# Optimization experiments

Measured on AMD Instinct MI355X. Metric: run time of the kernel, lower is better.

## Reference

```python
import jax, jax.numpy as jnp
import numpy as np
from jax import lax

WIN = 9
PAD = WIN // 2


def _box_sum(x):
    # x: [B,1,H,W]; all-ones WINxWIN conv, stride 1, pad PAD -> same spatial size
    k = jnp.ones((1, 1, WIN, WIN), dtype=x.dtype)
    return lax.conv_general_dilated(
        x, k, window_strides=(1, 1), padding=[(PAD, PAD), (PAD, PAD)],
        dimension_numbers=("NCHW", "OIHW", "NCHW"))


def setup_inputs() -> dict:
    key = jax.random.key(0)
    k1, k2 = jax.random.split(key)
    B, C, H, W = 32, 1, 512, 512
    y_true = jax.random.uniform(k1, (B, C, H, W), dtype=jnp.float32)
    y_pred = jax.random.uniform(k2, (B, C, H, W), dtype=jnp.float32)
    return {"y_true": y_true, "y_pred": y_pred}


def reference(y_true, y_pred):
    Ii, Ji = y_true, y_pred
    win_size = float(WIN * WIN)
    I_sum = _box_sum(Ii)
    J_sum = _box_sum(Ji)
    I2_sum = _box_sum(Ii * Ii)
    J2_sum = _box_sum(Ji * Ji)
    IJ_sum = _box_sum(Ii * Ji)
    u_I = I_sum / win_size
    u_J = J_sum / win_size
    cross = IJ_sum - u_J * I_sum - u_I * J_sum + u_I * u_J * win_size
    I_var = I2_sum - 2.0 * u_I * I_sum + u_I * u_I * win_size
    J_var = J2_sum - 2.0 * u_J * J_sum + u_J * u_J * win_size
    cc = cross * cross / (I_var * J_var + 1e-05)
    return -jnp.mean(cc)
```

## Files before the change

### kernel.cpp

```cpp
#include <hip/hip_runtime.h>


#define BATCH   32
#define IMH     512
#define IMW     512
#define SH      16
#define NSTRIP  32
#define NPART   (BATCH * NSTRIP)
#define NK      24
#define VROW    520

#define PREFG(KK, PI, PJ) do {                                             \
    const int kk_ = (KK);                                                  \
    const int ri_ = r0 - 4 + kk_;                                          \
    PI = make_float2(0.f, 0.f); PJ = make_float2(0.f, 0.f);                \
    if (kk_ < NK && (unsigned)ri_ < (unsigned)IMH) {                       \
        PI = *(const float2*)(Ib + (size_t)ri_ * IMW + c0);                \
        PJ = *(const float2*)(Jb + (size_t)ri_ * IMW + c0);                \
    }                                                                      \
} while (0)

#define HWIN(QI, HA, HB) do {                                              \
    const float2 w0_ = *(const float2*)&Vbuf[QI][c0];                      \
    const float2 w1_ = *(const float2*)&Vbuf[QI][c0 + 2];                  \
    const float2 w2_ = *(const float2*)&Vbuf[QI][c0 + 4];                  \
    const float2 w3_ = *(const float2*)&Vbuf[QI][c0 + 6];                  \
    const float2 w4_ = *(const float2*)&Vbuf[QI][c0 + 8];                  \
    HA = ((w0_.x + w0_.y) + (w1_.x + w1_.y))                               \
       + ((w2_.x + w2_.y) + (w3_.x + w3_.y)) + w4_.x;                      \
    HB = HA + w4_.y - w0_.x;                                               \
} while (0)

#define CC1(AI, AJ, S2, S3, S4) do {                                       \
    const float cross = (S4) - (AI)*(AJ)*inv81;                            \
    const float ivv   = (S2) - (AI)*(AI)*inv81;                            \
    const float jvv   = (S3) - (AJ)*(AJ)*inv81;                            \
    acc += cross * cross * __builtin_amdgcn_rcpf(ivv * jvv + 1e-5f);       \
} while (0)

#define EMIT() do {                                                        \
    *(float2*)&Vbuf[0][4 + c0] = make_float2(VI0, VI1);                    \
    *(float2*)&Vbuf[1][4 + c0] = make_float2(VJ0, VJ1);                    \
    *(float2*)&Vbuf[2][4 + c0] = make_float2(VA0, VA1);                    \
    *(float2*)&Vbuf[3][4 + c0] = make_float2(VB0, VB1);                    \
    *(float2*)&Vbuf[4][4 + c0] = make_float2(VC0, VC1);                    \
    __syncthreads();                                                       \
    float HI0, HI1, HJ0, HJ1, HA0, HA1, HB0, HB1, HC0, HC1;                \
    HWIN(0, HI0, HI1);                                                     \
    HWIN(1, HJ0, HJ1);                                                     \
    HWIN(2, HA0, HA1);                                                     \
    HWIN(3, HB0, HB1);                                                     \
    HWIN(4, HC0, HC1);                                                     \
    CC1(HI0, HJ0, HA0, HB0, HC0);                                          \
    CC1(HI1, HJ1, HA1, HB1, HC1);                                          \
    __syncthreads();      \
} while (0)

#define BODY(K, PI, PJ) do {                                               \
    float4 oldv = make_float4(0.f, 0.f, 0.f, 0.f);                         \
    if ((K) >= 9) oldv = ring[slot][t];                                    \
    ring[slot][t] = make_float4(PI.x, PI.y, PJ.x, PJ.y);                   \
    slot = (slot == 8) ? 0 : slot + 1;                                     \
    VI0 += PI.x - oldv.x;             VI1 += PI.y - oldv.y;                \
    VJ0 += PJ.x - oldv.z;             VJ1 += PJ.y - oldv.w;                \
    VA0 += PI.x*PI.x - oldv.x*oldv.x; VA1 += PI.y*PI.y - oldv.y*oldv.y;    \
    VB0 += PJ.x*PJ.x - oldv.z*oldv.z; VB1 += PJ.y*PJ.y - oldv.w*oldv.w;    \
    VC0 += PI.x*PJ.x - oldv.x*oldv.z; VC1 += PI.y*PJ.y - oldv.y*oldv.w;    \
    if ((K) >= 8) { EMIT(); }                                              \
} while (0)

__global__ __launch_bounds__(256, 4) void ncc_main(const float* __restrict__ I,
                                                   const float* __restrict__ J,
                                                   float* __restrict__ partial) {
    const int t  = threadIdx.x;
    const int s  = blockIdx.x;
    const int b  = blockIdx.y;
    const int r0 = s * SH;
    const int c0 = 2 * t;
    const float inv81 = 1.0f / 81.0f;

    const float* Ib = I + (size_t)b * IMH * IMW;
    const float* Jb = J + (size_t)b * IMH * IMW;

    __shared__ float  Vbuf[5][VROW];
    __shared__ float4 ring[9][256];

    if (t < 40) {
        const int q = t >> 3, p = t & 7;
        Vbuf[q][p < 4 ? p : 512 + p] = 0.f;
    }
    __syncthreads();

    float VI0 = 0.f, VI1 = 0.f, VJ0 = 0.f, VJ1 = 0.f;
    float VA0 = 0.f, VA1 = 0.f, VB0 = 0.f, VB1 = 0.f;
    float VC0 = 0.f, VC1 = 0.f;
    float acc = 0.f;
    int slot = 0;

    float2 pa_i, pa_j, pb_i, pb_j, pc_i, pc_j, pd_i, pd_j;
    PREFG(0, pa_i, pa_j);
    PREFG(1, pb_i, pb_j);
    PREFG(2, pc_i, pc_j);
    PREFG(3, pd_i, pd_j);

#pragma unroll 1
    for (int g = 0; g < 6; ++g) {
        const int K = 4 * g;
        BODY(K,     pa_i, pa_j);  PREFG(K + 4, pa_i, pa_j);
        BODY(K + 1, pb_i, pb_j);  PREFG(K + 5, pb_i, pb_j);
        BODY(K + 2, pc_i, pc_j);  PREFG(K + 6, pc_i, pc_j);
        BODY(K + 3, pd_i, pd_j);  PREFG(K + 7, pd_i, pd_j);
    }

    float sum = acc;
#pragma unroll
    for (int off = 32; off > 0; off >>= 1) sum += __shfl_down(sum, off, 64);

    __shared__ float wsum[4];
    if ((t & 63) == 0) wsum[t >> 6] = sum;
    __syncthreads();
    if (t == 0) {
        partial[(size_t)b * NSTRIP + s] = wsum[0] + wsum[1] + wsum[2] + wsum[3];
    }
}

__global__ __launch_bounds__(256) void ncc_reduce(const float* __restrict__ partial,
                                                  float* __restrict__ out) {
    const int t = threadIdx.x;
    double ssum = 0.0;
    for (int idx = t; idx < NPART; idx += 256) ssum += (double)partial[idx];
#pragma unroll
    for (int off = 32; off > 0; off >>= 1) ssum += __shfl_down(ssum, off, 64);

    __shared__ double wsum[4];
    if ((t & 63) == 0) wsum[t >> 6] = ssum;
    __syncthreads();
    if (t == 0) {
        const double total = wsum[0] + wsum[1] + wsum[2] + wsum[3];
        out[0] = (float)(-total / 8388608.0);
    }
}

extern "C" void kernel_launch(void* const* d_in, const int* in_sizes, int n_in,
                              void* d_out, int out_size, void* d_ws, size_t ws_size,
                              hipStream_t stream) {
    const float* I = (const float*)d_in[0];
    const float* J = (const float*)d_in[1];
    float* partial = (float*)d_ws;
    float* out     = (float*)d_out;

    dim3 grid(NSTRIP, BATCH);
    ncc_main<<<grid, 256, 0, stream>>>(I, J, partial);
    ncc_reduce<<<1, 256, 0, stream>>>(partial, out);
}
```

Baseline: 117.3 us.

## Use single-wavefront blocks with shuffle-based horizontal box sums

Each block becomes one 64-lane wavefront where every lane owns 8 contiguous columns. The horizontal 9-tap window sums are now built from per-lane prefix and suffix sums plus cross-lane shuffles, replacing the shared-memory staging buffer and the two block barriers per output row. Global loads widen to float4. The trade-off is only 1024 single-wave blocks, which means lower occupancy and less latency hiding, higher register pressure, and a prefetch depth cut from 4 rows to 2.

```diff
diff --git a/kernel.cpp b/kernel.cpp
--- a/kernel.cpp
+++ b/kernel.cpp
@@ -1,126 +1,152 @@
 #include <hip/hip_runtime.h>
 
 
-#define BATCH   32
-#define IMH     512
-#define IMW     512
-#define SH      16
-#define NSTRIP  32
-#define NPART   (BATCH * NSTRIP)
-#define NK      24
-#define VROW    520
+#define BATCH     32
+#define IMH       512
+#define IMW       512
+#define SH        16
+#define NROWSTRIP 32
+#define NK        (SH + 8)
+#define NPART     (BATCH * NROWSTRIP)
 
-#define PREFG(KK, PI, PJ) do {                                             \
+#define PREFG(KK, ILO, IHI, JLO, JHI) do {                                 \
     const int kk_ = (KK);                                                  \
     const int ri_ = r0 - 4 + kk_;                                          \
-    PI = make_float2(0.f, 0.f); PJ = make_float2(0.f, 0.f);                \
+    ILO = z4; IHI = z4; JLO = z4; JHI = z4;                                \
     if (kk_ < NK && (unsigned)ri_ < (unsigned)IMH) {                       \
-        PI = *(const float2*)(Ib + (size_t)ri_ * IMW + c0);                \
-        PJ = *(const float2*)(Jb + (size_t)ri_ * IMW + c0);                \
+        const float* rI_ = Ib + (size_t)ri_ * IMW + c0;                    \
+        const float* rJ_ = Jb + (size_t)ri_ * IMW + c0;                    \
+        ILO = *(const float4*)(rI_);                                       \
+        IHI = *(const float4*)(rI_ + 4);                                   \
+        JLO = *(const float4*)(rJ_);                                       \
+        JHI = *(const float4*)(rJ_ + 4);                                   \
     }                                                                      \
 } while (0)
 
-#define HWIN(QI, HA, HB) do {                                              \
-    const float2 w0_ = *(const float2*)&Vbuf[QI][c0];                      \
-    const float2 w1_ = *(const float2*)&Vbuf[QI][c0 + 2];                  \
-    const float2 w2_ = *(const float2*)&Vbuf[QI][c0 + 4];                  \
-    const float2 w3_ = *(const float2*)&Vbuf[QI][c0 + 6];                  \
-    const float2 w4_ = *(const float2*)&Vbuf[QI][c0 + 8];                  \
-    HA = ((w0_.x + w0_.y) + (w1_.x + w1_.y))                               \
-       + ((w2_.x + w2_.y) + (w3_.x + w3_.y)) + w4_.x;                      \
-    HB = HA + w4_.y - w0_.x;                                               \
+#define HQ(LO, HI_, H0, H1, H2, H3, H4, H5, H6, H7) do {                   \
+    const float P0 = (LO).x, P1 = P0 + (LO).y,                             \
+                P2 = P1 + (LO).z, P3 = P2 + (LO).w;                        \
+    const float P4 = P3 + (HI_).x, P5 = P4 + (HI_).y,                      \
+                P6 = P5 + (HI_).z, P7 = P6 + (HI_).w;                      \
+    const float S1 = (HI_).w, S2 = (HI_).z + S1,                           \
+                S3 = (HI_).y + S2, S4 = (HI_).x + S3;                      \
+    float ls4 = __shfl(S4, u - 1, 64), ls3 = __shfl(S3, u - 1, 64);        \
+    float ls2 = __shfl(S2, u - 1, 64), ls1 = __shfl(S1, u - 1, 64);        \
+    float rp1 = __shfl(P0, u + 1, 64), rp2 = __shfl(P1, u + 1, 64);        \
+    float rp3 = __shfl(P2, u + 1, 64), rp4 = __shfl(P3, u + 1, 64);        \
+    if (u == 0)  { ls4 = 0.f; ls3 = 0.f; ls2 = 0.f; ls1 = 0.f; }           \
+    if (u == 63) { rp1 = 0.f; rp2 = 0.f; rp3 = 0.f; rp4 = 0.f; }           \
+    H0 = ls4 + P4;        H1 = ls3 + P5;                                   \
+    H2 = ls2 + P6;        H3 = ls1 + P7;                                   \
+    H4 = P7 + rp1;        H5 = (P7 - P0) + rp2;                            \
+    H6 = (P7 - P1) + rp3; H7 = (P7 - P2) + rp4;                            \
 } while (0)
 
-#define CC1(AI, AJ, S2, S3, S4) do {                                       \
-    const float cross = (S4) - (AI)*(AJ)*inv81;                            \
-    const float ivv   = (S2) - (AI)*(AI)*inv81;                            \
-    const float jvv   = (S3) - (AJ)*(AJ)*inv81;                            \
-    acc += cross * cross * __builtin_amdgcn_rcpf(ivv * jvv + 1e-5f);       \
+#define ADD4(V, N, O) do {                                                 \
+    V.x += (N).x - (O).x; V.y += (N).y - (O).y;                            \
+    V.z += (N).z - (O).z; V.w += (N).w - (O).w; } while (0)
+#define ADDSQ4(V, N, O) do {                                               \
+    V.x += (N).x*(N).x - (O).x*(O).x; V.y += (N).y*(N).y - (O).y*(O).y;    \
+    V.z += (N).z*(N).z - (O).z*(O).z; V.w += (N).w*(N).w - (O).w*(O).w;    \
+} while (0)
+#define ADDPR4(V, NI, NJ, OI, OJ) do {                                     \
+    V.x += (NI).x*(NJ).x - (OI).x*(OJ).x;                                  \
+    V.y += (NI).y*(NJ).y - (OI).y*(OJ).y;                                  \
+    V.z += (NI).z*(NJ).z - (OI).z*(OJ).z;                                  \
+    V.w += (NI).w*(NJ).w - (OI).w*(OJ).w; } while (0)
+
+#define CCK(CR, IV, JV)                                                    \
+    acc += (CR) * (CR) * __builtin_amdgcn_rcpf((IV) * (JV) + 1e-5f)
+
+#define EMIT() do {                                                        \
+    float hI0,hI1,hI2,hI3,hI4,hI5,hI6,hI7;                                 \
+    float hJ0,hJ1,hJ2,hJ3,hJ4,hJ5,hJ6,hJ7;                                 \
+    HQ(VIlo, VIhi, hI0,hI1,hI2,hI3,hI4,hI5,hI6,hI7);                       \
+    HQ(VJlo, VJhi, hJ0,hJ1,hJ2,hJ3,hJ4,hJ5,hJ6,hJ7);                       \
+    const float x10=hI0*hJ0*inv81, x11=hI1*hJ1*inv81, x12=hI2*hJ2*inv81,   \
+                x13=hI3*hJ3*inv81, x14=hI4*hJ4*inv81, x15=hI5*hJ5*inv81,   \
+                x16=hI6*hJ6*inv81, x17=hI7*hJ7*inv81;                      \
+    const float x20=hI0*hI0*inv81, x21=hI1*hI1*inv81, x22=hI2*hI2*inv81,   \
+                x23=hI3*hI3*inv81, x24=hI4*hI4*inv81, x25=hI5*hI5*inv81,   \
+                x26=hI6*hI6*inv81, x27=hI7*hI7*inv81;                      \
+    const float x30=hJ0*hJ0*inv81, x31=hJ1*hJ1*inv81, x32=hJ2*hJ2*inv81,   \
+                x33=hJ3*hJ3*inv81, x34=hJ4*hJ4*inv81, x35=hJ5*hJ5*inv81,   \
+                x36=hJ6*hJ6*inv81, x37=hJ7*hJ7*inv81;                      \
+    float hA0,hA1,hA2,hA3,hA4,hA5,hA6,hA7;                                 \
+    HQ(VAlo, VAhi, hA0,hA1,hA2,hA3,hA4,hA5,hA6,hA7);                       \
+    const float iv0=hA0-x20, iv1=hA1-x21, iv2=hA2-x22, iv3=hA3-x23;        \
+    const float iv4=hA4-x24, iv5=hA5-x25, iv6=hA6-x26, iv7=hA7-x27;        \
+    float hB0,hB1,hB2,hB3,hB4,hB5,hB6,hB7;                                 \
+    HQ(VBlo, VBhi, hB0,hB1,hB2,hB3,hB4,hB5,hB6,hB7);                       \
+    const float jv0=hB0-x30, jv1=hB1-x31, jv2=hB2-x32, jv3=hB3-x33;        \
+    const float jv4=hB4-x34, jv5=hB5-x35, jv6=hB6-x36, jv7=hB7-x37;        \
+    float hC0,hC1,hC2,hC3,hC4,hC5,hC6,hC7;                                 \
+    HQ(VClo, VChi, hC0,hC1,hC2,hC3,hC4,hC5,hC6,hC7);                       \
+    CCK(hC0-x10, iv0, jv0); CCK(hC1-x11, iv1, jv1);                        \
+    CCK(hC2-x12, iv2, jv2); CCK(hC3-x13, iv3, jv3);                        \
+    CCK(hC4-x14, iv4, jv4); CCK(hC5-x15, iv5, jv5);                        \
+    CCK(hC6-x16, iv6, jv6); CCK(hC7-x17, iv7, jv7);                        \
 } while (0)
 
-#define EMIT() do {                                                        \
-    *(float2*)&Vbuf[0][4 + c0] = make_float2(VI0, VI1);                    \
-    *(float2*)&Vbuf[1][4 + c0] = make_float2(VJ0, VJ1);                    \
-    *(float2*)&Vbuf[2][4 + c0] = make_float2(VA0, VA1);                    \
-    *(float2*)&Vbuf[3][4 + c0] = make_float2(VB0, VB1);                    \
-    *(float2*)&Vbuf[4][4 + c0] = make_float2(VC0, VC1);                    \
-    __syncthreads();                                                       \
-    float HI0, HI1, HJ0, HJ1, HA0, HA1, HB0, HB1, HC0, HC1;                \
-    HWIN(0, HI0, HI1);                                                     \
-    HWIN(1, HJ0, HJ1);                                                     \
-    HWIN(2, HA0, HA1);                                                     \
-    HWIN(3, HB0, HB1);                                                     \
-    HWIN(4, HC0, HC1);                                                     \
-    CC1(HI0, HJ0, HA0, HB0, HC0);                                          \
-    CC1(HI1, HJ1, HA1, HB1, HC1);                                          \
-    __syncthreads();      \
-} while (0)
-
-#define BODY(K, PI, PJ) do {                                               \
-    float4 oldv = make_float4(0.f, 0.f, 0.f, 0.f);                         \
-    if ((K) >= 9) oldv = ring[slot][t];                                    \
-    ring[slot][t] = make_float4(PI.x, PI.y, PJ.x, PJ.y);                   \
+#define BODY(K, ILO, IHI, JLO, JHI) do {                                   \
+    float4 oIlo = z4, oIhi = z4, oJlo = z4, oJhi = z4;                     \
+    if ((K) >= 9) {                                                        \
+        oIlo = ringI[slot][u][0]; oIhi = ringI[slot][u][1];                \
+        oJlo = ringJ[slot][u][0]; oJhi = ringJ[slot][u][1];                \
+    }                                                                      \
+    ringI[slot][u][0] = ILO; ringI[slot][u][1] = IHI;                      \
+    ringJ[slot][u][0] = JLO; ringJ[slot][u][1] = JHI;                      \
     slot = (slot == 8) ? 0 : slot + 1;                                     \
-    VI0 += PI.x - oldv.x;             VI1 += PI.y - oldv.y;                \
-    VJ0 += PJ.x - oldv.z;             VJ1 += PJ.y - oldv.w;                \
-    VA0 += PI.x*PI.x - oldv.x*oldv.x; VA1 += PI.y*PI.y - oldv.y*oldv.y;    \
-    VB0 += PJ.x*PJ.x - oldv.z*oldv.z; VB1 += PJ.y*PJ.y - oldv.w*oldv.w;    \
-    VC0 += PI.x*PJ.x - oldv.x*oldv.z; VC1 += PI.y*PJ.y - oldv.y*oldv.w;    \
+    ADD4(VIlo, ILO, oIlo);          ADD4(VIhi, IHI, oIhi);                 \
+    ADD4(VJlo, JLO, oJlo);          ADD4(VJhi, JHI, oJhi);                 \
+    ADDSQ4(VAlo, ILO, oIlo);        ADDSQ4(VAhi, IHI, oIhi);               \
+    ADDSQ4(VBlo, JLO, oJlo);        ADDSQ4(VBhi, JHI, oJhi);               \
+    ADDPR4(VClo, ILO, JLO, oIlo, oJlo);                                    \
+    ADDPR4(VChi, IHI, JHI, oIhi, oJhi);                                    \
     if ((K) >= 8) { EMIT(); }                                              \
 } while (0)
 
-__global__ __launch_bounds__(256, 4) void ncc_main(const float* __restrict__ I,
-                                                   const float* __restrict__ J,
-                                                   float* __restrict__ partial) {
-    const int t  = threadIdx.x;
+__global__ __launch_bounds__(64, 1) void ncc_main(const float* __restrict__ I,
+                                                  const float* __restrict__ J,
+                                                  float* __restrict__ partial) {
+    const int u  = threadIdx.x;
     const int s  = blockIdx.x;
     const int b  = blockIdx.y;
     const int r0 = s * SH;
-    const int c0 = 2 * t;
+    const int c0 = 8 * u;
     const float inv81 = 1.0f / 81.0f;
+    const float4 z4 = make_float4(0.f, 0.f, 0.f, 0.f);
 
     const float* Ib = I + (size_t)b * IMH * IMW;
     const float* Jb = J + (size_t)b * IMH * IMW;
 
-    __shared__ float  Vbuf[5][VROW];
-    __shared__ float4 ring[9][256];
+    __shared__ float4 ringI[9][64][2];
+    __shared__ float4 ringJ[9][64][2];
 
-    if (t < 40) {
-        const int q = t >> 3, p = t & 7;
-        Vbuf[q][p < 4 ? p : 512 + p] = 0.f;
-    }
-    __syncthreads();
-
-    float VI0 = 0.f, VI1 = 0.f, VJ0 = 0.f, VJ1 = 0.f;
-    float VA0 = 0.f, VA1 = 0.f, VB0 = 0.f, VB1 = 0.f;
-    float VC0 = 0.f, VC1 = 0.f;
+    float4 VIlo = z4, VIhi = z4, VJlo = z4, VJhi = z4;
+    float4 VAlo = z4, VAhi = z4, VBlo = z4, VBhi = z4;
+    float4 VClo = z4, VChi = z4;
     float acc = 0.f;
     int slot = 0;
 
-    float2 pa_i, pa_j, pb_i, pb_j, pc_i, pc_j, pd_i, pd_j;
-    PREFG(0, pa_i, pa_j);
-    PREFG(1, pb_i, pb_j);
-    PREFG(2, pc_i, pc_j);
-    PREFG(3, pd_i, pd_j);
+    float4 aIlo, aIhi, aJlo, aJhi, bIlo, bIhi, bJlo, bJhi;
+    PREFG(0, aIlo, aIhi, aJlo, aJhi);
+    PREFG(1, bIlo, bIhi, bJlo, bJhi);
 
 #pragma unroll 1
-    for (int g = 0; g < 6; ++g) {
-        const int K = 4 * g;
-        BODY(K,     pa_i, pa_j);  PREFG(K + 4, pa_i, pa_j);
-        BODY(K + 1, pb_i, pb_j);  PREFG(K + 5, pb_i, pb_j);
-        BODY(K + 2, pc_i, pc_j);  PREFG(K + 6, pc_i, pc_j);
-        BODY(K + 3, pd_i, pd_j);  PREFG(K + 7, pd_i, pd_j);
+    for (int g = 0; g < NK / 2; ++g) {
+        const int K = 2 * g;
+        BODY(K,     aIlo, aIhi, aJlo, aJhi);
+        PREFG(K + 2, aIlo, aIhi, aJlo, aJhi);
+        BODY(K + 1, bIlo, bIhi, bJlo, bJhi);
+        PREFG(K + 3, bIlo, bIhi, bJlo, bJhi);
     }
 
     float sum = acc;
 #pragma unroll
     for (int off = 32; off > 0; off >>= 1) sum += __shfl_down(sum, off, 64);
-
-    __shared__ float wsum[4];
-    if ((t & 63) == 0) wsum[t >> 6] = sum;
-    __syncthreads();
-    if (t == 0) {
-        partial[(size_t)b * NSTRIP + s] = wsum[0] + wsum[1] + wsum[2] + wsum[3];
+    if (u == 0) {
+        partial[(size_t)b * NROWSTRIP + s] = sum;
     }
 }
 
@@ -149,7 +175,7 @@
     float* partial = (float*)d_ws;
     float* out     = (float*)d_out;
 
-    dim3 grid(NSTRIP, BATCH);
-    ncc_main<<<grid, 256, 0, stream>>>(I, J, partial);
+    dim3 grid(NROWSTRIP, BATCH);
+    ncc_main<<<grid, 64, 0, stream>>>(I, J, partial);
     ncc_reduce<<<1, 256, 0, stream>>>(partial, out);
 }
```

Measured after the change: 110.5 us. 5.8% less time.
